# Kernel tuning notes

Hardware: AMD Instinct MI355X
Metric: run time of the kernel (lower is better)

Reference implementation:

```python
import jax, jax.numpy as jnp
import numpy as np

B, SV, SA, D, H, L, F = 1, 2048, 512, 1024, 16, 2, 4096
DH = D // H
S = SV + SA


def layer_norm(x):
    mu = jnp.mean(x, axis=-1, keepdims=True)
    var = jnp.var(x, axis=-1, keepdims=True)
    return (x - mu) * jax.lax.rsqrt(var + 1e-6)


def rms_norm(x, g):
    return x * jax.lax.rsqrt(jnp.mean(x * x, axis=-1, keepdims=True) + 1e-6) * g


def rope(x, theta):
    # x: [B,S,H*DH], theta: [S, DH//2] angles; complex-pair rotation as in rope_apply
    b, s, _ = x.shape
    x4 = x.reshape(b, s, H, DH)
    xe, xo = x4[..., 0::2], x4[..., 1::2]
    c = jnp.cos(theta)[None, :, None, :]
    sn = jnp.sin(theta)[None, :, None, :]
    re = xe * c - xo * sn
    im = xe * sn + xo * c
    return jnp.stack([re, im], axis=-1).reshape(b, s, H * DH)


def setup_inputs() -> dict:
    key = jax.random.key(0)
    ks = jax.random.split(key, 20)
    w = 0.02
    inp = {
        'video_tokens': jax.random.normal(ks[0], (B, SV, D), jnp.float32),
        'action_tokens': jax.random.normal(ks[1], (B, SA, D), jnp.float32),
        'video_freqs': jax.random.uniform(ks[2], (SV, DH // 2), jnp.float32) * 6.28,
        'action_freqs': jax.random.uniform(ks[3], (SA, DH // 2), jnp.float32) * 6.28,
        'video_t_mod': jax.random.normal(ks[4], (B, 6, D), jnp.float32),
        'action_t_mod': jax.random.normal(ks[5], (B, 6, D), jnp.float32),
        'Wq': jax.random.normal(ks[6], (2, L, D, D), jnp.float32) * w,
        'Wk': jax.random.normal(ks[7], (2, L, D, D), jnp.float32) * w,
        'Wv': jax.random.normal(ks[8], (2, L, D, D), jnp.float32) * w,
        'Wo': jax.random.normal(ks[9], (2, L, D, D), jnp.float32) * w,
        'bq': jnp.zeros((2, L, D), jnp.float32),
        'bk': jnp.zeros((2, L, D), jnp.float32),
        'bv': jnp.zeros((2, L, D), jnp.float32),
        'bo': jnp.zeros((2, L, D), jnp.float32),
        'gq': jnp.ones((2, L, D), jnp.float32),
        'gk': jnp.ones((2, L, D), jnp.float32),
        'mod': jax.random.normal(ks[10], (2, L, 6, D), jnp.float32) * 0.02,
        'W1': jax.random.normal(ks[11], (2, L, D, F), jnp.float32) * w,
        'b1': jnp.zeros((2, L, F), jnp.float32),
        'W2': jax.random.normal(ks[12], (2, L, F, D), jnp.float32) * w,
        'b2': jnp.zeros((2, L, D), jnp.float32),
    }
    # Mixed-modality ctx_mask: video bidirectional; action attends video + causal over action
    m = np.zeros((S, S), dtype=bool)
    m[:SV, :SV] = True
    m[SV:, :SV] = True
    m[SV:, SV:] = np.tril(np.ones((SA, SA), dtype=bool))
    inp['attention_mask'] = jnp.asarray(m)
    return inp


def _mot_forward(video_tokens, action_tokens, video_freqs, action_freqs,
                 video_t_mod, action_t_mod, Wq, Wk, Wv, Wo, bq, bk, bv, bo,
                 gq, gk, mod, W1, b1, W2, b2, attention_mask):
    xs = [video_tokens, action_tokens]
    thetas = [video_freqs, action_freqs]
    tmods = [video_t_mod, action_t_mod]
    scale = 1.0 / jnp.sqrt(jnp.asarray(DH, xs[0].dtype))
    for l in range(L):
        qs, kss, vs, posts = [], [], [], []
        for e in range(2):
            m6 = mod[e, l][None] + tmods[e]  # [B,6,D]
            sh_msa, sc_msa, g_msa, sh_mlp, sc_mlp, g_mlp = (
                m6[:, i:i + 1, :] for i in range(6))
            a = layer_norm(xs[e]) * (1.0 + sc_msa) + sh_msa
            q = rope(rms_norm(a @ Wq[e, l] + bq[e, l], gq[e, l]), thetas[e])
            k = rope(rms_norm(a @ Wk[e, l] + bk[e, l], gk[e, l]), thetas[e])
            v = a @ Wv[e, l] + bv[e, l]
            qs.append(q); kss.append(k); vs.append(v)
            posts.append((g_msa, sh_mlp, sc_mlp, g_mlp))
        qc = jnp.concatenate(qs, axis=1).reshape(B, S, H, DH)
        kc = jnp.concatenate(kss, axis=1).reshape(B, S, H, DH)
        vc = jnp.concatenate(vs, axis=1).reshape(B, S, H, DH)
        scores = jnp.einsum('bqhd,bkhd->bhqk', qc, kc) * scale
        scores = jnp.where(attention_mask[None, None], scores, -1e9)
        p = jax.nn.softmax(scores, axis=-1)
        o = jnp.einsum('bhqk,bkhd->bqhd', p, vc).reshape(B, S, H * DH)
        outs = [o[:, :SV], o[:, SV:]]
        for e in range(2):
            g_msa, sh_mlp, sc_mlp, g_mlp = posts[e]
            x = xs[e] + g_msa * (outs[e] @ Wo[e, l] + bo[e, l])
            mi = layer_norm(x) * (1.0 + sc_mlp) + sh_mlp
            h = jax.nn.gelu(mi @ W1[e, l] + b1[e, l], approximate=True) @ W2[e, l] + b2[e, l]
            xs[e] = x + g_mlp * h
    return jnp.concatenate(xs, axis=1)  # [B, SV+SA, D]


def reference(video_tokens, action_tokens, video_freqs, action_freqs,
              video_t_mod, action_t_mod, Wq, Wk, Wv, Wo, bq, bk, bv, bo,
              gq, gk, mod, W1, b1, W2, b2, attention_mask):
    return _mot_forward(video_tokens, action_tokens, video_freqs, action_freqs,
                        video_t_mod, action_t_mod, Wq, Wk, Wv, Wo, bq, bk, bv, bo,
                        gq, gk, mod, W1, b1, W2, b2, attention_mask)
```

## Files before the change

kernel.cpp:

```cpp
#include <hip/hip_runtime.h>
#include <hip/hip_bf16.h>

#define BF16 __hip_bfloat16
typedef short bf16x8 __attribute__((ext_vector_type(8)));
typedef float f32x4  __attribute__((ext_vector_type(4)));
typedef unsigned int u32;

#define MFMA16(a, b, c) __builtin_amdgcn_mfma_f32_16x16x32_bf16(a, b, c, 0, 0, 0)


__device__ __forceinline__ void async16(const void* g, void* l) {
  __builtin_amdgcn_global_load_lds(
      (const __attribute__((address_space(1))) u32*)g,
      (__attribute__((address_space(3))) u32*)l, 16, 0, 0);
}

__device__ __forceinline__ u32 pkbf(float a, float b) {
  union { BF16 h; unsigned short s; } ua, ub;
  ua.h = __float2bfloat16(a); ub.h = __float2bfloat16(b);
  return (u32)ua.s | ((u32)ub.s << 16);
}

__device__ __forceinline__ float bf2f(short s) {
  union { float f; u32 u; } v;
  v.u = ((u32)(unsigned short)s) << 16;
  return v.f;
}

__global__ __launch_bounds__(256) void wtrans(const float* __restrict__ W,
                                              BF16* __restrict__ WT, int K, int N,
                                              size_t outZ) {
  __shared__ float t[32][33];
  const float* Wm = W + (size_t)K * N * blockIdx.z;
  BF16* Tm = WT + outZ * blockIdx.z;
  int n0 = blockIdx.x * 32, k0 = blockIdx.y * 32;
  int tx = threadIdx.x & 31, ty = threadIdx.x >> 5;
#pragma unroll
  for (int i = 0; i < 4; i++)
    t[ty + 8 * i][tx] = Wm[(size_t)(k0 + ty + 8 * i) * N + n0 + tx];
  __syncthreads();
#pragma unroll
  for (int i = 0; i < 4; i++)
    Tm[(size_t)(n0 + ty + 8 * i) * K + k0 + tx] = __float2bfloat16(t[tx][ty + 8 * i]);
}

__global__ __launch_bounds__(256) void wtransq(const float* __restrict__ Wq,
                                               const float* __restrict__ Wk,
                                               const float* __restrict__ Wv,
                                               BF16* __restrict__ WT) {
  __shared__ float t[32][33];
  int mat = blockIdx.z >> 2, ex = blockIdx.z & 3;
  const float* Wm = (mat == 0 ? Wq : mat == 1 ? Wk : Wv) + (size_t)ex * 1024 * 1024;
  BF16* Tm = WT + (size_t)ex * 3072 * 1024 + (size_t)mat * 1024 * 1024;
  int n0 = blockIdx.x * 32, k0 = blockIdx.y * 32;
  int tx = threadIdx.x & 31, ty = threadIdx.x >> 5;
#pragma unroll
  for (int i = 0; i < 4; i++)
    t[ty + 8 * i][tx] = Wm[(size_t)(k0 + ty + 8 * i) * 1024 + n0 + tx];
  __syncthreads();
#pragma unroll
  for (int i = 0; i < 4; i++)
    Tm[(size_t)(n0 + ty + 8 * i) * 1024 + k0 + tx] = __float2bfloat16(t[tx][ty + 8 * i]);
}

__global__ __launch_bounds__(256) void packb(const float* __restrict__ bq,
                                             const float* __restrict__ bk,
                                             const float* __restrict__ bv,
                                             float* __restrict__ bqkv) {
  int i = blockIdx.x * 256 + threadIdx.x;
  int s = i / 3072, c = i - s * 3072;
  float v = (c < 1024) ? bq[s * 1024 + c]
          : (c < 2048) ? bk[s * 1024 + c - 1024]
                       : bv[s * 1024 + c - 2048];
  bqkv[i] = v;
}

__global__ __launch_bounds__(256) void ln_mod(const float* __restrict__ xV,
                                              const float* __restrict__ xA,
                                              BF16* __restrict__ out,
                                              const float* __restrict__ mod,
                                              const float* __restrict__ tmv,
                                              const float* __restrict__ tma,
                                              int l, int ish, int isc) {
  int r = blockIdx.x;
  int e = (r >= 2048) ? 1 : 0;
  const float* xrow = e ? (xA + (size_t)(r - 2048) * 1024) : (xV + (size_t)r * 1024);
  const float* tm = e ? tma : tmv;
  const float* mo = mod + (size_t)((e * 2 + l) * 6) * 1024;
  float4 v = ((const float4*)xrow)[threadIdx.x];
  float s = v.x + v.y + v.z + v.w;
  float s2 = v.x * v.x + v.y * v.y + v.z * v.z + v.w * v.w;
#pragma unroll
  for (int off = 32; off >= 1; off >>= 1) {
    s += __shfl_down(s, off);
    s2 += __shfl_down(s2, off);
  }
  __shared__ float red[8];
  int lane = threadIdx.x & 63, w = threadIdx.x >> 6;
  if (lane == 0) { red[w] = s; red[4 + w] = s2; }
  __syncthreads();
  s = red[0] + red[1] + red[2] + red[3];
  s2 = red[4] + red[5] + red[6] + red[7];
  float mu = s * (1.f / 1024.f);
  float var = s2 * (1.f / 1024.f) - mu * mu;
  float inv = rsqrtf(var + 1e-6f);
  int c = threadIdx.x * 4;
  BF16* o = out + (size_t)r * 1024 + c;
  float xv[4] = {v.x, v.y, v.z, v.w};
#pragma unroll
  for (int k = 0; k < 4; k++) {
    float sc = mo[isc * 1024 + c + k] + tm[isc * 1024 + c + k];
    float sh = mo[ish * 1024 + c + k] + tm[ish * 1024 + c + k];
    o[k] = __float2bfloat16((xv[k] - mu) * inv * (1.f + sc) + sh);
  }
}

__global__ __launch_bounds__(256) void qk_post(const float* __restrict__ qkv,
                                               const float* __restrict__ gq,
                                               const float* __restrict__ gk,
                                               BF16* __restrict__ Qb, BF16* __restrict__ Kb,
                                               const float* __restrict__ vfreq,
                                               const float* __restrict__ afreq, int l) {
  int r = blockIdx.x;
  int which = blockIdx.y;
  const float* src = qkv + (size_t)r * 3072 + which * 1024;
  int e = (r >= 2048) ? 1 : 0;
  const float* g = (which ? gk : gq) + (size_t)(e * 2 + l) * 1024;
  BF16* dst = which ? Kb : Qb;
  const float* fr = e ? (afreq + (size_t)(r - 2048) * 32) : (vfreq + (size_t)r * 32);
  float4 v = ((const float4*)src)[threadIdx.x];
  float s2 = v.x * v.x + v.y * v.y + v.z * v.z + v.w * v.w;
#pragma unroll
  for (int off = 32; off >= 1; off >>= 1) s2 += __shfl_down(s2, off);
  __shared__ float red[4];
  int lane = threadIdx.x & 63, w = threadIdx.x >> 6;
  if (lane == 0) red[w] = s2;
  __syncthreads();
  s2 = red[0] + red[1] + red[2] + red[3];
  float inv = rsqrtf(s2 * (1.f / 1024.f) + 1e-6f);
  if (which == 0) inv *= 0.125f * 1.44269504f;
  int c = threadIdx.x * 4;
  float xe0 = v.x * inv * g[c], xo0 = v.y * inv * g[c + 1];
  float xe1 = v.z * inv * g[c + 2], xo1 = v.w * inv * g[c + 3];
  int p0 = (c & 63) >> 1;
  float c0, s0, c1, s1;
  __sincosf(fr[p0], &s0, &c0);
  __sincosf(fr[p0 + 1], &s1, &c1);
  int h = c >> 6;
  size_t o = ((size_t)h * 2560 + r) * 64 + (c & 63);
  dst[o + 0] = __float2bfloat16(xe0 * c0 - xo0 * s0);
  dst[o + 1] = __float2bfloat16(xe0 * s0 + xo0 * c0);
  dst[o + 2] = __float2bfloat16(xe1 * c1 - xo1 * s1);
  dst[o + 3] = __float2bfloat16(xe1 * s1 + xo1 * c1);
}

__global__ __launch_bounds__(256) void vpost(const float* __restrict__ qkv,
                                             BF16* __restrict__ VT) {
  __shared__ float t[32][33];
  int r0 = blockIdx.x * 32, c0 = blockIdx.y * 32;
  int tx = threadIdx.x & 31, ty = threadIdx.x >> 5;
#pragma unroll
  for (int i = 0; i < 4; i++)
    t[ty + 8 * i][tx] = qkv[(size_t)(r0 + ty + 8 * i) * 3072 + 2048 + c0 + tx];
  __syncthreads();
#pragma unroll
  for (int i = 0; i < 4; i++)
    VT[(size_t)(c0 + ty + 8 * i) * 2560 + r0 + tx] = __float2bfloat16(t[tx][ty + 8 * i]);
}

template <int EPI, int KS>
__global__ __launch_bounds__(256) void gemm2(const BF16* __restrict__ A,
                                             const BF16* __restrict__ Bw, size_t Bestride,
                                             const float* __restrict__ bias, int biasE,
                                             void* __restrict__ out, float* __restrict__ part,
                                             int N, int K) {
  __shared__ BF16 As[128 * 64];
  __shared__ BF16 Bs[128 * 64];
  int flat = blockIdx.x + blockIdx.y * gridDim.x;
  int xcd = flat & 7, slot = flat >> 3;
  int bx = slot % gridDim.x;
  int by = (slot / gridDim.x) * 8 + xcd;
  int m0 = bx * 128, n0 = by * 128;
  int e = (m0 >= 2048);
  const BF16* Ab = A + (size_t)m0 * K;
  const BF16* Bb = Bw + (e ? Bestride : 0) + (size_t)n0 * K;
  int kz0 = blockIdx.z * (K / KS), kz1 = kz0 + K / KS;
  int tid = threadIdx.x, lane = tid & 63, w = tid >> 6;
  int wr = w & 1, wc = w >> 1;
  int m15 = lane & 15, q4 = lane >> 4;
  int L[4], rS[4], cS[4];
#pragma unroll
  for (int i = 0; i < 4; i++) {
    L[i] = w * 256 + i * 64 + lane;
    rS[i] = L[i] >> 3;
    cS[i] = (L[i] & 7) ^ (rS[i] & 7);
  }
  f32x4 acc[4][4] = {};
  for (int k0 = kz0; k0 < kz1; k0 += 64) {
    __syncthreads();
#pragma unroll
    for (int i = 0; i < 4; i++) {
      async16(Ab + (size_t)rS[i] * K + k0 + cS[i] * 8, &As[L[i] * 8]);
      async16(Bb + (size_t)rS[i] * K + k0 + cS[i] * 8, &Bs[L[i] * 8]);
    }
    __syncthreads();
#pragma unroll
    for (int kk = 0; kk < 2; kk++) {
      int pos = ((kk * 4 + q4) ^ (m15 & 7)) * 8;
      bf16x8 af[4], bv[4];
#pragma unroll
      for (int i = 0; i < 4; i++) af[i] = *(const bf16x8*)&As[(wr * 64 + i * 16 + m15) * 64 + pos];
#pragma unroll
      for (int j = 0; j < 4; j++) bv[j] = *(const bf16x8*)&Bs[(wc * 64 + j * 16 + m15) * 64 + pos];
#pragma unroll
      for (int i = 0; i < 4; i++)
#pragma unroll
        for (int j = 0; j < 4; j++)
          acc[i][j] = MFMA16(af[i], bv[j], acc[i][j]);
    }
  }
#pragma unroll
  for (int i = 0; i < 4; i++) {
    int row = m0 + wr * 64 + 16 * i + q4 * 4;
#pragma unroll
    for (int j = 0; j < 4; j++) {
      int col = n0 + wc * 64 + 16 * j + m15;
      float b = (EPI == 3) ? 0.f : bias[e * biasE + col];
#pragma unroll
      for (int rg = 0; rg < 4; rg++) {
        float v = acc[i][j][rg] + b;
        size_t idx = (size_t)(row + rg) * N + col;
        if (EPI == 0) {
          ((float*)out)[idx] = v;
        } else if (EPI == 1) {
          float u = v * (0.7978845608f + 0.0356774081f * v * v);
          float d = 1.f + exp2f(-2.8853900818f * u);
          ((BF16*)out)[idx] = __float2bfloat16(v * __builtin_amdgcn_rcpf(d));
        } else {
          part[(size_t)blockIdx.z * 2560 * N + idx] = v;
        }
      }
    }
  }
}

template <int KS, int LN>
__global__ __launch_bounds__(256) void combine_ln(const float* __restrict__ part,
                                                  const float* __restrict__ biasL,
                                                  const float* __restrict__ modp,
                                                  int gi, int lg, int ll, int ish, int isc,
                                                  const float* __restrict__ tmv,
                                                  const float* __restrict__ tma,
                                                  const float* __restrict__ xinV,
                                                  const float* __restrict__ xinA,
                                                  float* __restrict__ xout,
                                                  BF16* __restrict__ lnout) {
  int r = blockIdx.x, e = (r >= 2048) ? 1 : 0;
  int c = threadIdx.x * 4;
  float4 s = {0.f, 0.f, 0.f, 0.f};
#pragma unroll
  for (int z = 0; z < KS; z++) {
    float4 p = *(const float4*)&part[((size_t)z * 2560 + r) * 1024 + c];
    s.x += p.x; s.y += p.y; s.z += p.z; s.w += p.w;
  }
  float4 b = *(const float4*)&biasL[e * 2048 + c];
  const float* tm = e ? tma : tmv;
  float4 gm = *(const float4*)&modp[(size_t)((e * 2 + lg) * 6 + gi) * 1024 + c];
  float4 gt = *(const float4*)&tm[gi * 1024 + c];
  const float* xrow = e ? (xinA + (size_t)(r - 2048) * 1024) : (xinV + (size_t)r * 1024);
  float4 xi = *(const float4*)&xrow[c];
  float4 o;
  o.x = xi.x + (gm.x + gt.x) * (s.x + b.x);
  o.y = xi.y + (gm.y + gt.y) * (s.y + b.y);
  o.z = xi.z + (gm.z + gt.z) * (s.z + b.z);
  o.w = xi.w + (gm.w + gt.w) * (s.w + b.w);
  *(float4*)&xout[(size_t)r * 1024 + c] = o;
  if (LN) {
    float su = o.x + o.y + o.z + o.w;
    float s2 = o.x * o.x + o.y * o.y + o.z * o.z + o.w * o.w;
#pragma unroll
    for (int off = 32; off >= 1; off >>= 1) {
      su += __shfl_down(su, off);
      s2 += __shfl_down(s2, off);
    }
    __shared__ float red[8];
    int lane = threadIdx.x & 63, w = threadIdx.x >> 6;
    if (lane == 0) { red[w] = su; red[4 + w] = s2; }
    __syncthreads();
    su = red[0] + red[1] + red[2] + red[3];
    s2 = red[4] + red[5] + red[6] + red[7];
    float mu = su * (1.f / 1024.f);
    float var = s2 * (1.f / 1024.f) - mu * mu;
    float inv = rsqrtf(var + 1e-6f);
    const float* mo = modp + (size_t)((e * 2 + ll) * 6) * 1024;
    BF16* ob = lnout + (size_t)r * 1024 + c;
    float ov[4] = {o.x, o.y, o.z, o.w};
#pragma unroll
    for (int k = 0; k < 4; k++) {
      float sc = mo[isc * 1024 + c + k] + tm[isc * 1024 + c + k];
      float sh = mo[ish * 1024 + c + k] + tm[ish * 1024 + c + k];
      ob[k] = __float2bfloat16((ov[k] - mu) * inv * (1.f + sc) + sh);
    }
  }
}

__global__ __launch_bounds__(256) void flash6(const BF16* __restrict__ Qb,
                                              const BF16* __restrict__ Kb,
                                              const BF16* __restrict__ VT,
                                              BF16* __restrict__ Opb,
                                              float* __restrict__ ml) {
  const int S = 2560;
  const size_t ZOb = 16ull * 40 * 4096;
  const size_t ZM = 16ull * 40 * 128;
  __shared__ BF16 Ks[2][64 * 64];
  __shared__ BF16 Vs[2][64 * 64];
  __shared__ BF16 Ps[4][16 * 64];
  int tid = threadIdx.x, lane = tid & 63, w = tid >> 6;
  int h = blockIdx.y, q0 = blockIdx.x * 64, kz = blockIdx.z;
  int m15 = lane & 15, q4 = lane >> 4;
  int actq = (q0 >= 2048);
  int nt = actq ? ((q0 >> 6) + 1) : 32;
  int tb = (kz * nt) >> 2, te = ((kz + 1) * nt) >> 2;
  const BF16* qrow = Qb + ((size_t)h * S + q0 + w * 16 + m15) * 64;
  bf16x8 qf0 = *(const bf16x8*)(qrow + q4 * 8);
  bf16x8 qf1 = *(const bf16x8*)(qrow + 32 + q4 * 8);
  const BF16* kbase = Kb + (size_t)h * S * 64;
  const BF16* vbase = VT + (size_t)h * 64 * S;
  int L0 = w * 128 + lane, L1 = L0 + 64;
  int r0 = L0 >> 3, c0 = (L0 & 7) ^ (r0 & 7);
  int r1 = L1 >> 3, c1 = (L1 & 7) ^ (r1 & 7);
  {
    const BF16* kg = kbase + (size_t)tb * 64 * 64;
    const BF16* vg = vbase + (size_t)tb * 64;
    async16(kg + (size_t)r0 * 64 + c0 * 8, &Ks[0][L0 * 8]);
    async16(kg + (size_t)r1 * 64 + c1 * 8, &Ks[0][L1 * 8]);
    async16(vg + (size_t)r0 * S + c0 * 8, &Vs[0][L0 * 8]);
    async16(vg + (size_t)r1 * S + c1 * 8, &Vs[0][L1 * 8]);
  }
  f32x4 oa[4] = {};
  float m_i = -1e30f, l_i = 0.f;
  int colq = q0 + w * 16 + m15;
  char* Pw = (char*)&Ps[w][0];
  int prow = m15 * 128;
  int pswz = (m15 & 7) << 4;
  int x0 = (q4 ^ (m15 & 7)) * 8, x1 = ((4 + q4) ^ (m15 & 7)) * 8;
  __syncthreads();
  for (int t = tb; t < te; t++) {
    int cur = (t - tb) & 1;
    if (t + 1 < te) {
      int nb = cur ^ 1;
      const BF16* kg = kbase + (size_t)(t + 1) * 64 * 64;
      const BF16* vg = vbase + (size_t)(t + 1) * 64;
      async16(kg + (size_t)r0 * 64 + c0 * 8, &Ks[nb][L0 * 8]);
      async16(kg + (size_t)r1 * 64 + c1 * 8, &Ks[nb][L1 * 8]);
      async16(vg + (size_t)r0 * S + c0 * 8, &Vs[nb][L0 * 8]);
      async16(vg + (size_t)r1 * S + c1 * 8, &Vs[nb][L1 * 8]);
    }
    f32x4 st[4];
    __builtin_amdgcn_s_setprio(1);
#pragma unroll
    for (int jt = 0; jt < 4; jt++) {
      int row = (jt * 16 + m15) * 64;
      bf16x8 kf0 = *(const bf16x8*)&Ks[cur][row + x0];
      bf16x8 kf1 = *(const bf16x8*)&Ks[cur][row + x1];
      f32x4 zz = {};
      zz = MFMA16(kf0, qf0, zz);
      st[jt] = MFMA16(kf1, qf1, zz);
    }
    __builtin_amdgcn_s_setprio(0);
    float mx = -1e30f;
    if (actq && t == nt - 1) {
#pragma unroll
      for (int jt = 0; jt < 4; jt++)
#pragma unroll
        for (int rg = 0; rg < 4; rg++) {
          int rowkv = t * 64 + jt * 16 + q4 * 4 + rg;
          if (rowkv > colq) st[jt][rg] = -1e30f;
          mx = fmaxf(mx, st[jt][rg]);
        }
    } else {
#pragma unroll
      for (int jt = 0; jt < 4; jt++) {
        mx = fmaxf(fmaxf(mx, st[jt][0]), st[jt][1]);
        mx = fmaxf(fmaxf(mx, st[jt][2]), st[jt][3]);
      }
    }
    if (!__all(mx <= m_i + 8.f)) {
      float m2 = fmaxf(mx, __shfl_xor(mx, 16));
      m2 = fmaxf(m2, __shfl_xor(m2, 32));
      float mn = fmaxf(m_i, m2);
      float al = exp2f(m_i - mn);
      m_i = mn;
      l_i *= al;
      float alr[4];
#pragma unroll
      for (int rg = 0; rg < 4; rg++) alr[rg] = __shfl(al, q4 * 4 + rg);
#pragma unroll
      for (int dt = 0; dt < 4; dt++)
#pragma unroll
        for (int rg = 0; rg < 4; rg++) oa[dt][rg] *= alr[rg];
    }
    float rs = 0.f;
#pragma unroll
    for (int jt = 0; jt < 4; jt++) {
      float p0 = exp2f(st[jt][0] - m_i), p1 = exp2f(st[jt][1] - m_i);
      float p2 = exp2f(st[jt][2] - m_i), p3 = exp2f(st[jt][3] - m_i);
      rs += (p0 + p1) + (p2 + p3);
      uint2 pr = {pkbf(p0, p1), pkbf(p2, p3)};
      *(uint2*)(Pw + prow + ((jt * 32 + q4 * 8) ^ pswz)) = pr;
    }
    l_i += rs;
    bf16x8 pf0 = *(const bf16x8*)(Pw + prow + ((q4 * 16) ^ pswz));
    bf16x8 pf1 = *(const bf16x8*)(Pw + prow + ((64 + q4 * 16) ^ pswz));
    __builtin_amdgcn_s_setprio(1);
#pragma unroll
    for (int dt = 0; dt < 4; dt++) {
      int vr = (dt * 16 + m15) * 64;
      bf16x8 vf0 = *(const bf16x8*)&Vs[cur][vr + x0];
      bf16x8 vf1 = *(const bf16x8*)&Vs[cur][vr + x1];
      oa[dt] = MFMA16(pf0, vf0, oa[dt]);
      oa[dt] = MFMA16(pf1, vf1, oa[dt]);
    }
    __builtin_amdgcn_s_setprio(0);
    __syncthreads();
  }
  l_i += __shfl_xor(l_i, 16);
  l_i += __shfl_xor(l_i, 32);
  if (q4 == 0) {
    float* mp = ml + (size_t)kz * ZM + ((size_t)h * 40 + blockIdx.x) * 128;
    mp[w * 16 + m15] = m_i;
    mp[64 + w * 16 + m15] = l_i;
  }
  BF16* rp = &Ks[0][0];
#pragma unroll
  for (int dt = 0; dt < 4; dt++)
#pragma unroll
    for (int rg = 0; rg < 4; rg++)
      rp[(w * 16 + q4 * 4 + rg) * 72 + dt * 16 + m15] = __float2bfloat16(oa[dt][rg]);
  __syncthreads();
  BF16* Opz = Opb + (size_t)kz * ZOb + ((size_t)h * 40 + blockIdx.x) * 4096;
#pragma unroll
  for (int kk = 0; kk < 2; kk++) {
    int k = tid * 2 + kk;
    int row = k >> 3, ci = k & 7;
    uint4 d = *(const uint4*)&rp[row * 72 + ci * 8];
    *(uint4*)&Opz[(size_t)row * 64 + ci * 8] = d;
  }
}

__global__ __launch_bounds__(256) void fcomb4b(const BF16* __restrict__ Opb,
                                               const float* __restrict__ ml,
                                               BF16* __restrict__ O) {
  int qt = blockIdx.x, h = blockIdx.y;
  int q = threadIdx.x >> 2;
  int d0 = (threadIdx.x & 3) * 16;
  const size_t ZOb = 16ull * 40 * 4096;
  const size_t ZM = 16ull * 40 * 128;
  size_t tile = (size_t)h * 40 + qt;
  size_t base = tile * 4096 + (size_t)q * 64 + d0;
  size_t mb = tile * 128 + q;
  float m[4], lv[4];
#pragma unroll
  for (int z = 0; z < 4; z++) {
    m[z] = ml[z * ZM + mb];
    lv[z] = ml[z * ZM + mb + 64];
  }
  float M = fmaxf(fmaxf(m[0], m[1]), fmaxf(m[2], m[3]));
  float wz[4];
  float den = 0.f;
#pragma unroll
  for (int z = 0; z < 4; z++) {
    wz[z] = exp2f(m[z] - M);
    den += wz[z] * lv[z];
  }
  float r = 1.f / den;
#pragma unroll
  for (int z = 0; z < 4; z++) wz[z] *= r;
  float acc[16] = {};
#pragma unroll
  for (int z = 0; z < 4; z++) {
    const BF16* P = Opb + z * ZOb + base;
    bf16x8 a = *(const bf16x8*)P;
    bf16x8 b = *(const bf16x8*)(P + 8);
#pragma unroll
    for (int i = 0; i < 8; i++) {
      acc[i] += wz[z] * bf2f(a[i]);
      acc[8 + i] += wz[z] * bf2f(b[i]);
    }
  }
  BF16* orow = O + (size_t)(qt * 64 + q) * 1024 + h * 64 + d0;
  u32 pk[8];
#pragma unroll
  for (int i = 0; i < 8; i++) pk[i] = pkbf(acc[2 * i], acc[2 * i + 1]);
  *(uint4*)&orow[0] = *(uint4*)&pk[0];
  *(uint4*)&orow[8] = *(uint4*)&pk[4];
}

extern "C" void kernel_launch(void* const* d_in, const int* in_sizes, int n_in,
                              void* d_out, int out_size, void* d_ws, size_t ws_size,
                              hipStream_t stream) {
  (void)in_sizes; (void)n_in; (void)out_size; (void)ws_size;
  const float* vid  = (const float*)d_in[0];
  const float* act  = (const float*)d_in[1];
  const float* vfr  = (const float*)d_in[2];
  const float* afr  = (const float*)d_in[3];
  const float* tmv  = (const float*)d_in[4];
  const float* tma  = (const float*)d_in[5];
  const float* Wq   = (const float*)d_in[6];
  const float* Wk   = (const float*)d_in[7];
  const float* Wv   = (const float*)d_in[8];
  const float* Wo   = (const float*)d_in[9];
  const float* bq   = (const float*)d_in[10];
  const float* bk   = (const float*)d_in[11];
  const float* bv   = (const float*)d_in[12];
  const float* bo   = (const float*)d_in[13];
  const float* gq   = (const float*)d_in[14];
  const float* gk   = (const float*)d_in[15];
  const float* modp = (const float*)d_in[16];
  const float* W1   = (const float*)d_in[17];
  const float* b1   = (const float*)d_in[18];
  const float* W2   = (const float*)d_in[19];
  const float* b2   = (const float*)d_in[20];

  char* p = (char*)d_ws;
  auto carve = [&](size_t bytes) {
    char* r = p;
    p += (bytes + 255) & ~(size_t)255;
    return r;
  };
  BF16* WqkvT = (BF16*)carve(4ull * 3072 * 1024 * 2);
  BF16* WoT   = (BF16*)carve(4ull * 1024 * 1024 * 2);
  BF16* W1T   = (BF16*)carve(4ull * 4096 * 1024 * 2);
  BF16* W2T   = (BF16*)carve(4ull * 1024 * 4096 * 2);
  float* bqkv = (float*)carve(4ull * 3072 * 4);
  float* x    = (float*)carve(2560ull * 1024 * 4);
  BF16* abf   = (BF16*)carve(2560ull * 1024 * 2);
  float* qkv  = (float*)carve(2560ull * 3072 * 4);
  BF16* Qb    = (BF16*)carve(2560ull * 1024 * 2);
  BF16* Kb    = (BF16*)carve(2560ull * 1024 * 2);
  float* part = qkv;
  const size_t ZOb = 16ull * 40 * 4096;
  BF16* Opb = (BF16*)qkv;
  float* mlb = (float*)((char*)qkv + 4ull * ZOb * 2);
  BF16* VTb   = (BF16*)carve(2560ull * 1024 * 2);
  BF16* Obf   = (BF16*)carve(2560ull * 1024 * 2);
  BF16* mibf  = (BF16*)carve(2560ull * 1024 * 2);
  BF16* hbf   = (BF16*)carve(2560ull * 4096 * 2);

  const size_t S3 = 3072ull * 1024;
  wtransq<<<dim3(32, 32, 12), 256, 0, stream>>>(Wq, Wk, Wv, WqkvT);
  wtrans<<<dim3(32, 32, 4), 256, 0, stream>>>(Wo, WoT, 1024, 1024, 1024ull * 1024);
  wtrans<<<dim3(128, 32, 4), 256, 0, stream>>>(W1, W1T, 1024, 4096, 4096ull * 1024);
  wtrans<<<dim3(32, 128, 4), 256, 0, stream>>>(W2, W2T, 4096, 1024, 1024ull * 4096);
  packb<<<48, 256, 0, stream>>>(bq, bk, bv, bqkv);

  ln_mod<<<2560, 256, 0, stream>>>(vid, act, abf, modp, tmv, tma, 0, 0, 1);

  for (int l = 0; l < 2; l++) {
    gemm2<0, 1><<<dim3(20, 24, 1), 256, 0, stream>>>(
        abf, WqkvT + (size_t)l * S3, 2 * S3, bqkv + l * 3072, 6144, qkv, nullptr, 3072, 1024);
    qk_post<<<dim3(2560, 2), 256, 0, stream>>>(qkv, gq, gk, Qb, Kb, vfr, afr, l);
    vpost<<<dim3(80, 32), 256, 0, stream>>>(qkv, VTb);
    flash6<<<dim3(40, 16, 4), 256, 0, stream>>>(Qb, Kb, VTb, Opb, mlb);
    fcomb4b<<<dim3(40, 16), 256, 0, stream>>>(Opb, mlb, Obf);
    gemm2<3, 2><<<dim3(20, 8, 2), 256, 0, stream>>>(
        Obf, WoT + (size_t)l * 1024 * 1024, 2ull * 1024 * 1024, nullptr, 0, nullptr, part,
        1024, 1024);
    combine_ln<2, 1><<<2560, 256, 0, stream>>>(
        part, bo + l * 1024, modp, 2, l, l, 3, 4, tmv, tma,
        (l == 0) ? vid : x, (l == 0) ? act : (x + 2048ull * 1024), x, mibf);
    gemm2<1, 1><<<dim3(20, 32, 1), 256, 0, stream>>>(
        mibf, W1T + (size_t)l * 4096 * 1024, 2ull * 4096 * 1024, b1 + l * 4096, 8192, hbf,
        nullptr, 4096, 1024);
    gemm2<3, 4><<<dim3(20, 8, 4), 256, 0, stream>>>(
        hbf, W2T + (size_t)l * 4096 * 1024, 2ull * 4096 * 1024, nullptr, 0, nullptr, part,
        1024, 4096);
    if (l == 0) {
      combine_ln<4, 1><<<2560, 256, 0, stream>>>(
          part, b2, modp, 5, 0, 1, 0, 1, tmv, tma, x, x + 2048ull * 1024, x, abf);
    } else {
      combine_ln<4, 0><<<2560, 256, 0, stream>>>(
          part, b2 + 1024, modp, 5, 1, 0, 0, 0, tmv, tma, x, x + 2048ull * 1024,
          (float*)d_out, nullptr);
    }
  }
}
```

Before: 750.9 us.

## Double-buffer GEMM LDS tiles and store split-K partials as bf16

The GEMM main loop now uses two LDS buffers per operand and issues the async global-to-LDS loads for the next K tile before computing the current one, with one barrier per iteration instead of two. This is meant to overlap memory latency with MFMA work. LDS use doubles to 64 KB per block, which can reduce occupancy. Split-K partial sums are also written and read as bf16 instead of fp32, halving the partial-buffer traffic at some accuracy cost. The code does not show a wait for the async loads before the barrier, so the pipeline depends on the barrier covering them.

```diff
diff --git a/kernel.cpp b/kernel.cpp
--- a/kernel.cpp
+++ b/kernel.cpp
@@ -172,10 +172,10 @@
 __global__ __launch_bounds__(256) void gemm2(const BF16* __restrict__ A,
                                              const BF16* __restrict__ Bw, size_t Bestride,
                                              const float* __restrict__ bias, int biasE,
-                                             void* __restrict__ out, float* __restrict__ part,
+                                             void* __restrict__ out, BF16* __restrict__ part,
                                              int N, int K) {
-  __shared__ BF16 As[128 * 64];
-  __shared__ BF16 Bs[128 * 64];
+  __shared__ BF16 As[2][128 * 64];
+  __shared__ BF16 Bs[2][128 * 64];
   int flat = blockIdx.x + blockIdx.y * gridDim.x;
   int xcd = flat & 7, slot = flat >> 3;
   int bx = slot % gridDim.x;
@@ -184,7 +184,8 @@
   int e = (m0 >= 2048);
   const BF16* Ab = A + (size_t)m0 * K;
   const BF16* Bb = Bw + (e ? Bestride : 0) + (size_t)n0 * K;
-  int kz0 = blockIdx.z * (K / KS), kz1 = kz0 + K / KS;
+  int kz0 = blockIdx.z * (K / KS);
+  int nk = (K / KS) >> 6;
   int tid = threadIdx.x, lane = tid & 63, w = tid >> 6;
   int wr = w & 1, wc = w >> 1;
   int m15 = lane & 15, q4 = lane >> 4;
@@ -196,28 +197,39 @@
     cS[i] = (L[i] & 7) ^ (rS[i] & 7);
   }
   f32x4 acc[4][4] = {};
-  for (int k0 = kz0; k0 < kz1; k0 += 64) {
-    __syncthreads();
-#pragma unroll
-    for (int i = 0; i < 4; i++) {
-      async16(Ab + (size_t)rS[i] * K + k0 + cS[i] * 8, &As[L[i] * 8]);
-      async16(Bb + (size_t)rS[i] * K + k0 + cS[i] * 8, &Bs[L[i] * 8]);
-    }
-    __syncthreads();
+#pragma unroll
+  for (int i = 0; i < 4; i++) {
+    async16(Ab + (size_t)rS[i] * K + kz0 + cS[i] * 8, &As[0][L[i] * 8]);
+    async16(Bb + (size_t)rS[i] * K + kz0 + cS[i] * 8, &Bs[0][L[i] * 8]);
+  }
+  __syncthreads();
+  for (int t = 0; t < nk; t++) {
+    int cur = t & 1, nb = cur ^ 1;
+    if (t + 1 < nk) {
+      int k0 = kz0 + (t + 1) * 64;
+#pragma unroll
+      for (int i = 0; i < 4; i++) {
+        async16(Ab + (size_t)rS[i] * K + k0 + cS[i] * 8, &As[nb][L[i] * 8]);
+        async16(Bb + (size_t)rS[i] * K + k0 + cS[i] * 8, &Bs[nb][L[i] * 8]);
+      }
+    }
 #pragma unroll
     for (int kk = 0; kk < 2; kk++) {
       int pos = ((kk * 4 + q4) ^ (m15 & 7)) * 8;
       bf16x8 af[4], bv[4];
 #pragma unroll
-      for (int i = 0; i < 4; i++) af[i] = *(const bf16x8*)&As[(wr * 64 + i * 16 + m15) * 64 + pos];
-#pragma unroll
-      for (int j = 0; j < 4; j++) bv[j] = *(const bf16x8*)&Bs[(wc * 64 + j * 16 + m15) * 64 + pos];
+      for (int i = 0; i < 4; i++)
+        af[i] = *(const bf16x8*)&As[cur][(wr * 64 + i * 16 + m15) * 64 + pos];
+#pragma unroll
+      for (int j = 0; j < 4; j++)
+        bv[j] = *(const bf16x8*)&Bs[cur][(wc * 64 + j * 16 + m15) * 64 + pos];
 #pragma unroll
       for (int i = 0; i < 4; i++)
 #pragma unroll
         for (int j = 0; j < 4; j++)
           acc[i][j] = MFMA16(af[i], bv[j], acc[i][j]);
     }
+    __syncthreads();
   }
 #pragma unroll
   for (int i = 0; i < 4; i++) {
@@ -237,7 +249,7 @@
           float d = 1.f + exp2f(-2.8853900818f * u);
           ((BF16*)out)[idx] = __float2bfloat16(v * __builtin_amdgcn_rcpf(d));
         } else {
-          part[(size_t)blockIdx.z * 2560 * N + idx] = v;
+          part[(size_t)blockIdx.z * 2560 * N + idx] = __float2bfloat16(v);
         }
       }
     }
@@ -245,7 +257,7 @@
 }
 
 template <int KS, int LN>
-__global__ __launch_bounds__(256) void combine_ln(const float* __restrict__ part,
+__global__ __launch_bounds__(256) void combine_ln(const BF16* __restrict__ part,
                                                   const float* __restrict__ biasL,
                                                   const float* __restrict__ modp,
                                                   int gi, int lg, int ll, int ish, int isc,
@@ -260,8 +272,8 @@
   float4 s = {0.f, 0.f, 0.f, 0.f};
 #pragma unroll
   for (int z = 0; z < KS; z++) {
-    float4 p = *(const float4*)&part[((size_t)z * 2560 + r) * 1024 + c];
-    s.x += p.x; s.y += p.y; s.z += p.z; s.w += p.w;
+    short4 p4 = *(const short4*)&part[((size_t)z * 2560 + r) * 1024 + c];
+    s.x += bf2f(p4.x); s.y += bf2f(p4.y); s.z += bf2f(p4.z); s.w += bf2f(p4.w);
   }
   float4 b = *(const float4*)&biasL[e * 2048 + c];
   const float* tm = e ? tma : tmv;
@@ -538,7 +550,7 @@
   float* qkv  = (float*)carve(2560ull * 3072 * 4);
   BF16* Qb    = (BF16*)carve(2560ull * 1024 * 2);
   BF16* Kb    = (BF16*)carve(2560ull * 1024 * 2);
-  float* part = qkv;
+  BF16* part = (BF16*)qkv;
   const size_t ZOb = 16ull * 40 * 4096;
   BF16* Opb = (BF16*)qkv;
   float* mlb = (float*)((char*)qkv + 4ull * ZOb * 2);
```

Result: no change. 741.7 us (-1.2%).

## Halve GEMM N-tile to 64 and store split-K partials in bf16

Applied to the files above, without the earlier changes.

Shrinks the gemm2 output tile from 128x128 to 128x64 and doubles the grid along N, so more blocks run on the 256 CUs and less LDS is used per block. Split-K partial sums are now written as bf16 instead of fp32, halving partial-buffer traffic; combine_ln converts them back on load. The trade-off is lower arithmetic intensity per block (more A reloads), and rounding each partial to bf16 before summation loses precision.

```diff
diff --git a/kernel.cpp b/kernel.cpp
--- a/kernel.cpp
+++ b/kernel.cpp
@@ -172,15 +172,15 @@
 __global__ __launch_bounds__(256) void gemm2(const BF16* __restrict__ A,
                                              const BF16* __restrict__ Bw, size_t Bestride,
                                              const float* __restrict__ bias, int biasE,
-                                             void* __restrict__ out, float* __restrict__ part,
+                                             void* __restrict__ out, BF16* __restrict__ part,
                                              int N, int K) {
   __shared__ BF16 As[128 * 64];
-  __shared__ BF16 Bs[128 * 64];
+  __shared__ BF16 Bs[64 * 64];
   int flat = blockIdx.x + blockIdx.y * gridDim.x;
   int xcd = flat & 7, slot = flat >> 3;
   int bx = slot % gridDim.x;
   int by = (slot / gridDim.x) * 8 + xcd;
-  int m0 = bx * 128, n0 = by * 128;
+  int m0 = bx * 128, n0 = by * 64;
   int e = (m0 >= 2048);
   const BF16* Ab = A + (size_t)m0 * K;
   const BF16* Bb = Bw + (e ? Bestride : 0) + (size_t)n0 * K;
@@ -188,34 +188,44 @@
   int tid = threadIdx.x, lane = tid & 63, w = tid >> 6;
   int wr = w & 1, wc = w >> 1;
   int m15 = lane & 15, q4 = lane >> 4;
-  int L[4], rS[4], cS[4];
+  int LA[4], rA[4], cA[4];
 #pragma unroll
   for (int i = 0; i < 4; i++) {
-    L[i] = w * 256 + i * 64 + lane;
-    rS[i] = L[i] >> 3;
-    cS[i] = (L[i] & 7) ^ (rS[i] & 7);
-  }
-  f32x4 acc[4][4] = {};
+    LA[i] = w * 256 + i * 64 + lane;
+    rA[i] = LA[i] >> 3;
+    cA[i] = (LA[i] & 7) ^ (rA[i] & 7);
+  }
+  int LB[2], rB[2], cB[2];
+#pragma unroll
+  for (int i = 0; i < 2; i++) {
+    LB[i] = w * 128 + i * 64 + lane;
+    rB[i] = LB[i] >> 3;
+    cB[i] = (LB[i] & 7) ^ (rB[i] & 7);
+  }
+  f32x4 acc[4][2] = {};
   for (int k0 = kz0; k0 < kz1; k0 += 64) {
     __syncthreads();
 #pragma unroll
-    for (int i = 0; i < 4; i++) {
-      async16(Ab + (size_t)rS[i] * K + k0 + cS[i] * 8, &As[L[i] * 8]);
-      async16(Bb + (size_t)rS[i] * K + k0 + cS[i] * 8, &Bs[L[i] * 8]);
-    }
+    for (int i = 0; i < 4; i++)
+      async16(Ab + (size_t)rA[i] * K + k0 + cA[i] * 8, &As[LA[i] * 8]);
+#pragma unroll
+    for (int i = 0; i < 2; i++)
+      async16(Bb + (size_t)rB[i] * K + k0 + cB[i] * 8, &Bs[LB[i] * 8]);
     __syncthreads();
 #pragma unroll
     for (int kk = 0; kk < 2; kk++) {
       int pos = ((kk * 4 + q4) ^ (m15 & 7)) * 8;
-      bf16x8 af[4], bv[4];
-#pragma unroll
-      for (int i = 0; i < 4; i++) af[i] = *(const bf16x8*)&As[(wr * 64 + i * 16 + m15) * 64 + pos];
-#pragma unroll
-      for (int j = 0; j < 4; j++) bv[j] = *(const bf16x8*)&Bs[(wc * 64 + j * 16 + m15) * 64 + pos];
+      bf16x8 af[4], bv[2];
 #pragma unroll
       for (int i = 0; i < 4; i++)
-#pragma unroll
-        for (int j = 0; j < 4; j++)
+        af[i] = *(const bf16x8*)&As[(wr * 64 + i * 16 + m15) * 64 + pos];
+#pragma unroll
+      for (int j = 0; j < 2; j++)
+        bv[j] = *(const bf16x8*)&Bs[(wc * 32 + j * 16 + m15) * 64 + pos];
+#pragma unroll
+      for (int i = 0; i < 4; i++)
+#pragma unroll
+        for (int j = 0; j < 2; j++)
           acc[i][j] = MFMA16(af[i], bv[j], acc[i][j]);
     }
   }
@@ -223,8 +233,8 @@
   for (int i = 0; i < 4; i++) {
     int row = m0 + wr * 64 + 16 * i + q4 * 4;
 #pragma unroll
-    for (int j = 0; j < 4; j++) {
-      int col = n0 + wc * 64 + 16 * j + m15;
+    for (int j = 0; j < 2; j++) {
+      int col = n0 + wc * 32 + 16 * j + m15;
       float b = (EPI == 3) ? 0.f : bias[e * biasE + col];
 #pragma unroll
       for (int rg = 0; rg < 4; rg++) {
@@ -237,7 +247,7 @@
           float d = 1.f + exp2f(-2.8853900818f * u);
           ((BF16*)out)[idx] = __float2bfloat16(v * __builtin_amdgcn_rcpf(d));
         } else {
-          part[(size_t)blockIdx.z * 2560 * N + idx] = v;
+          part[(size_t)blockIdx.z * 2560 * N + idx] = __float2bfloat16(v);
         }
       }
     }
@@ -245,7 +255,7 @@
 }
 
 template <int KS, int LN>
-__global__ __launch_bounds__(256) void combine_ln(const float* __restrict__ part,
+__global__ __launch_bounds__(256) void combine_ln(const BF16* __restrict__ part,
                                                   const float* __restrict__ biasL,
                                                   const float* __restrict__ modp,
                                                   int gi, int lg, int ll, int ish, int isc,
@@ -260,8 +270,8 @@
   float4 s = {0.f, 0.f, 0.f, 0.f};
 #pragma unroll
   for (int z = 0; z < KS; z++) {
-    float4 p = *(const float4*)&part[((size_t)z * 2560 + r) * 1024 + c];
-    s.x += p.x; s.y += p.y; s.z += p.z; s.w += p.w;
+    short4 p4 = *(const short4*)&part[((size_t)z * 2560 + r) * 1024 + c];
+    s.x += bf2f(p4.x); s.y += bf2f(p4.y); s.z += bf2f(p4.z); s.w += bf2f(p4.w);
   }
   float4 b = *(const float4*)&biasL[e * 2048 + c];
   const float* tm = e ? tma : tmv;
@@ -538,7 +548,7 @@
   float* qkv  = (float*)carve(2560ull * 3072 * 4);
   BF16* Qb    = (BF16*)carve(2560ull * 1024 * 2);
   BF16* Kb    = (BF16*)carve(2560ull * 1024 * 2);
-  float* part = qkv;
+  BF16* part = (BF16*)qkv;
   const size_t ZOb = 16ull * 40 * 4096;
   BF16* Opb = (BF16*)qkv;
   float* mlb = (float*)((char*)qkv + 4ull * ZOb * 2);
@@ -557,22 +567,22 @@
   ln_mod<<<2560, 256, 0, stream>>>(vid, act, abf, modp, tmv, tma, 0, 0, 1);
 
   for (int l = 0; l < 2; l++) {
-    gemm2<0, 1><<<dim3(20, 24, 1), 256, 0, stream>>>(
+    gemm2<0, 1><<<dim3(20, 48, 1), 256, 0, stream>>>(
         abf, WqkvT + (size_t)l * S3, 2 * S3, bqkv + l * 3072, 6144, qkv, nullptr, 3072, 1024);
     qk_post<<<dim3(2560, 2), 256, 0, stream>>>(qkv, gq, gk, Qb, Kb, vfr, afr, l);
     vpost<<<dim3(80, 32), 256, 0, stream>>>(qkv, VTb);
     flash6<<<dim3(40, 16, 4), 256, 0, stream>>>(Qb, Kb, VTb, Opb, mlb);
     fcomb4b<<<dim3(40, 16), 256, 0, stream>>>(Opb, mlb, Obf);
-    gemm2<3, 2><<<dim3(20, 8, 2), 256, 0, stream>>>(
+    gemm2<3, 2><<<dim3(20, 16, 2), 256, 0, stream>>>(
         Obf, WoT + (size_t)l * 1024 * 1024, 2ull * 1024 * 1024, nullptr, 0, nullptr, part,
         1024, 1024);
     combine_ln<2, 1><<<2560, 256, 0, stream>>>(
         part, bo + l * 1024, modp, 2, l, l, 3, 4, tmv, tma,
         (l == 0) ? vid : x, (l == 0) ? act : (x + 2048ull * 1024), x, mibf);
-    gemm2<1, 1><<<dim3(20, 32, 1), 256, 0, stream>>>(
+    gemm2<1, 1><<<dim3(20, 64, 1), 256, 0, stream>>>(
         mibf, W1T + (size_t)l * 4096 * 1024, 2ull * 4096 * 1024, b1 + l * 4096, 8192, hbf,
         nullptr, 4096, 1024);
-    gemm2<3, 4><<<dim3(20, 8, 4), 256, 0, stream>>>(
+    gemm2<3, 4><<<dim3(20, 16, 4), 256, 0, stream>>>(
         hbf, W2T + (size_t)l * 4096 * 1024, 2ull * 4096 * 1024, nullptr, 0, nullptr, part,
         1024, 4096);
     if (l == 0) {
```

After: 718.4 us. 1.05x faster.
